# Performance work log

Measured on AMD Instinct MI355X. Metric: run time of the kernel, lower is better.

The kernel has to match this reference:

```python
import jax, jax.numpy as jnp
import numpy as np

N, C, T, H, W = 4, 512, 8, 28, 28
CQ, CV = C // 8, C // 2  # 64, 256


def _maxpool222(a):
    # max_pool3d with kernel=stride=(2,2,2), VALID, over (t,h,w) of [n,c,t,h,w]
    return jax.lax.reduce_window(a, -jnp.inf, jax.lax.max,
                                 (1, 1, 2, 2, 2), (1, 1, 2, 2, 2), 'VALID')


def setup_inputs() -> dict:
    key = jax.random.key(0)
    ks = jax.random.split(key, 6)
    s = lambda fan_in: 1.0 / np.sqrt(fan_in)
    return {
        'x':  jax.random.normal(ks[0], (N, C, T, H, W), dtype=jnp.float32),
        'Wq': jax.random.normal(ks[1], (CQ, C), dtype=jnp.float32) * s(C),
        'Wk': jax.random.normal(ks[2], (CQ, C), dtype=jnp.float32) * s(C),
        'Wv': jax.random.normal(ks[3], (CV, C), dtype=jnp.float32) * s(C),
        'Wz': jax.random.normal(ks[4], (C, CV), dtype=jnp.float32) * s(CV),
        'y':  jax.random.normal(ks[5], (), dtype=jnp.float32) * 0.1,
    }


def reference(x, Wq, Wk, Wv, Wz, y):
    n, c, t, h, w = x.shape
    # 1x1x1 convs (no bias) = per-voxel channel mixing
    q = jnp.einsum('ncthw,oc->nothw', x, Wq)          # [n, CQ, t, h, w]
    k = _maxpool222(jnp.einsum('ncthw,oc->nothw', x, Wk))  # [n, CQ, t/2, h/2, w/2]
    v = _maxpool222(jnp.einsum('ncthw,oc->nothw', x, Wv))  # [n, CV, t/2, h/2, w/2]

    Lq = t * h * w
    Lk = k.shape[2] * k.shape[3] * k.shape[4]
    qf = q.reshape(n, q.shape[1], Lq)                 # [n, CQ, Lq]
    kf = k.reshape(n, k.shape[1], Lk)                 # [n, CQ, Lk]
    vf = v.reshape(n, v.shape[1], Lk)                 # [n, CV, Lk]

    # beta = softmax(q^T k) over kv axis (NOTE: no 1/sqrt(d) scaling, as in source)
    beta = jax.nn.softmax(jnp.einsum('ncq,nck->nqk', qf, kf), axis=-1)  # [n, Lq, Lk]
    att = jnp.einsum('nck,nqk->ncq', vf, beta)        # [n, CV, Lq]
    att = att.reshape(n, vf.shape[1], t, h, w)

    z = jnp.einsum('ncthw,oc->nothw', att, Wz)        # [n, C, t, h, w]
    return y * z + x
```

## Files before the change

### kernel.cpp

```cpp
#include <hip/hip_runtime.h>
#include <hip/hip_bf16.h>

#define LSP  6272
#define LK   784
#define CIN  512
#define CQo  64
#define CVo  256
#define NB   4

typedef __bf16  bf16x8 __attribute__((ext_vector_type(8)));
typedef __bf16  bf16x4 __attribute__((ext_vector_type(4)));
typedef float   f32x4  __attribute__((ext_vector_type(4)));

#define LDT  40

__global__ __launch_bounds__(256) void xt_kernel(const float* __restrict__ x,
                                                 __bf16* __restrict__ xT)
{
    __shared__ __attribute__((aligned(16))) __bf16 tile[64][68];
    int t = threadIdx.x;
    int p0 = blockIdx.x * 64, c0 = blockIdx.y * 64, n = blockIdx.z;
    #pragma unroll
    for (int i = 0; i < 4; i++) {
        int idx = i * 256 + t;
        int c = idx >> 4, p4 = (idx & 15) * 4;
        const float4 v = *reinterpret_cast<const float4*>(
            &x[((size_t)(n * CIN + c0 + c)) * LSP + p0 + p4]);
        tile[p4 + 0][c] = (__bf16)v.x;
        tile[p4 + 1][c] = (__bf16)v.y;
        tile[p4 + 2][c] = (__bf16)v.z;
        tile[p4 + 3][c] = (__bf16)v.w;
    }
    __syncthreads();
    #pragma unroll
    for (int i = 0; i < 4; i++) {
        int idx = i * 256 + t;
        int p = idx >> 4, c4 = (idx & 15) * 4;
        bf16x4 o;
        o[0] = tile[p][c4 + 0]; o[1] = tile[p][c4 + 1];
        o[2] = tile[p][c4 + 2]; o[3] = tile[p][c4 + 3];
        *reinterpret_cast<bf16x4*>(&xT[((size_t)(n * LSP + p0 + p)) * CIN + c0 + c4]) = o;
    }
}

__global__ void wprep_kernel(const float* __restrict__ Wq, const float* __restrict__ Wk,
                             const float* __restrict__ Wv, const float* __restrict__ Wz,
                             __bf16* __restrict__ Wqkv, __bf16* __restrict__ Wzb)
{
    int idx = blockIdx.x * 256 + threadIdx.x;
    if (idx < 384 * 512) {
        int o = idx >> 9;
        float v = (o < 64) ? Wq[idx] : (o < 128) ? Wk[idx - 64 * 512] : Wv[idx - 128 * 512];
        Wqkv[idx] = (__bf16)v;
    }
    if (idx < 512 * 256) Wzb[idx] = (__bf16)Wz[idx];
}

__global__ __launch_bounds__(256) void qkv_gemm(const __bf16* __restrict__ Wqkv,
                                                const __bf16* __restrict__ xT,
                                                __bf16* __restrict__ qT,
                                                __bf16* __restrict__ kT,
                                                __bf16* __restrict__ vconv)
{
    __shared__ __attribute__((aligned(16))) __bf16 As[128 * LDT];
    __shared__ __attribute__((aligned(16))) __bf16 Bs[128 * LDT];
    int t = threadIdx.x;
    int p0 = blockIdx.x * 128;
    int m0 = blockIdx.y * 128;
    int n  = blockIdx.z;
    int lane = t & 63, wid = t >> 6;
    int wm = wid >> 1, wn = wid & 1;
    int lm = lane & 15, lk = lane >> 4;

    f32x4 acc[4][4] = {};

    for (int kb = 0; kb < CIN; kb += 32) {
        #pragma unroll
        for (int i = 0; i < 2; i++) {
            int idx = i * 2048 + t * 8;
            int r = idx >> 5, k8 = idx & 31;
            *reinterpret_cast<uint4*>(&As[r * LDT + k8]) =
                *reinterpret_cast<const uint4*>(&Wqkv[(size_t)(m0 + r) * CIN + kb + k8]);
            *reinterpret_cast<uint4*>(&Bs[r * LDT + k8]) =
                *reinterpret_cast<const uint4*>(&xT[((size_t)(n * LSP + p0 + r)) * CIN + kb + k8]);
        }
        __syncthreads();
        bf16x8 a[4], b[4];
        #pragma unroll
        for (int mi = 0; mi < 4; mi++)
            a[mi] = *reinterpret_cast<const bf16x8*>(&As[(wm * 64 + mi * 16 + lm) * LDT + lk * 8]);
        #pragma unroll
        for (int ni = 0; ni < 4; ni++)
            b[ni] = *reinterpret_cast<const bf16x8*>(&Bs[(wn * 64 + ni * 16 + lm) * LDT + lk * 8]);
        #pragma unroll
        for (int mi = 0; mi < 4; mi++)
            #pragma unroll
            for (int ni = 0; ni < 4; ni++)
                acc[mi][ni] = __builtin_amdgcn_mfma_f32_16x16x32_bf16(a[mi], b[ni], acc[mi][ni], 0, 0, 0);
        __syncthreads();
    }

    #pragma unroll
    for (int mi = 0; mi < 4; mi++) {
        int mloc = wm * 64 + mi * 16 + lk * 4;
        #pragma unroll
        for (int ni = 0; ni < 4; ni++) {
            int p = p0 + wn * 64 + ni * 16 + lm;
            if (m0 == 0) {
                bf16x4 o;
                o[0] = (__bf16)acc[mi][ni][0]; o[1] = (__bf16)acc[mi][ni][1];
                o[2] = (__bf16)acc[mi][ni][2]; o[3] = (__bf16)acc[mi][ni][3];
                if (mloc < 64)
                    *reinterpret_cast<bf16x4*>(&qT[((size_t)(n * LSP + p)) * 64 + mloc]) = o;
                else
                    *reinterpret_cast<bf16x4*>(&kT[((size_t)(n * LSP + p)) * 64 + (mloc - 64)]) = o;
            } else {
                int cv = m0 - 128 + mloc;
                #pragma unroll
                for (int r = 0; r < 4; r++)
                    vconv[((size_t)(n * CVo + cv + r)) * LSP + p] = (__bf16)acc[mi][ni][r];
            }
        }
    }
}

__global__ __launch_bounds__(256) void poolk_kernel(const __bf16* __restrict__ kT,
                                                    __bf16* __restrict__ kpT)
{
    int wid = threadIdx.x >> 6, lane = threadIdx.x & 63;
    int row = blockIdx.x * 4 + wid;
    int n = row / LK, pk = row % LK;
    int tp = pk / 196, rem = pk % 196, hp = rem / 14, wp = rem % 14;
    const __bf16* b = kT + ((size_t)n * LSP + tp * 2 * 784 + hp * 2 * 28 + wp * 2) * 64 + lane;
    float m =        (float)b[0];
    m = fmaxf(m, (float)b[64]);
    m = fmaxf(m, (float)b[28 * 64]);
    m = fmaxf(m, (float)b[29 * 64]);
    m = fmaxf(m, (float)b[784 * 64]);
    m = fmaxf(m, (float)b[785 * 64]);
    m = fmaxf(m, (float)b[812 * 64]);
    m = fmaxf(m, (float)b[813 * 64]);
    kpT[(size_t)row * 64 + lane] = (__bf16)m;
}

__global__ void poolv_kernel(const __bf16* __restrict__ vconv, __bf16* __restrict__ vp)
{
    int id = blockIdx.x * 256 + threadIdx.x;
    if (id >= NB * CVo * LK) return;
    int nc = id / LK, pk = id % LK;
    int tp = pk / 196, rem = pk % 196, hp = rem / 14, wp = rem % 14;
    const __bf16* b = vconv + (size_t)nc * LSP + tp * 2 * 784 + hp * 2 * 28 + wp * 2;
    float m =        (float)b[0];
    m = fmaxf(m, (float)b[1]);   m = fmaxf(m, (float)b[28]);  m = fmaxf(m, (float)b[29]);
    m = fmaxf(m, (float)b[784]); m = fmaxf(m, (float)b[785]); m = fmaxf(m, (float)b[812]); m = fmaxf(m, (float)b[813]);
    vp[id] = (__bf16)m;
}

__global__ __launch_bounds__(256) void flash_kernel(
    const __bf16* __restrict__ qT, const __bf16* __restrict__ kpT,
    const __bf16* __restrict__ vp, __bf16* __restrict__ attT)
{
    __shared__ __attribute__((aligned(16))) __bf16 Ps[64 * 128];
    __shared__ float smem_s[64];
    int t = threadIdx.x;
    int lane = t & 63, w = t >> 6;
    int lm = lane & 15, lk = lane >> 4;
    int q0 = blockIdx.x * 64;
    int n  = blockIdx.y;

    bf16x8 qa[2];
    {
        const __bf16* qrow = &qT[((size_t)(n * LSP + q0 + w * 16 + lm)) * 64 + lk * 8];
        qa[0] = *reinterpret_cast<const bf16x8*>(qrow);
        qa[1] = *reinterpret_cast<const bf16x8*>(qrow + 32);
    }

    f32x4 accO[4][4] = {};
    float m[4], l[4];
    #pragma unroll
    for (int r = 0; r < 4; r++) { m[r] = -1e30f; l[r] = 0.0f; }

    int qrow = w * 16 + lk * 4;

    for (int kt = 0; kt < 7; kt++) {
        int k0 = kt * 128;
        f32x4 accS[8] = {};
        #pragma unroll
        for (int ks = 0; ks < 2; ks++) {
            #pragma unroll
            for (int ni = 0; ni < 8; ni++) {
                int k = k0 + ni * 16 + lm; if (k > 783) k = 783;
                bf16x8 kb = *reinterpret_cast<const bf16x8*>(
                    &kpT[((size_t)(n * LK + k)) * 64 + ks * 32 + lk * 8]);
                accS[ni] = __builtin_amdgcn_mfma_f32_16x16x32_bf16(qa[ks], kb, accS[ni], 0, 0, 0);
            }
        }
        if (kt == 6) {
            #pragma unroll
            for (int ni = 1; ni < 8; ni++)
                #pragma unroll
                for (int r = 0; r < 4; r++) accS[ni][r] = -1e30f;
        }
        float scale[4], lt[4];
        #pragma unroll
        for (int r = 0; r < 4; r++) {
            float v = accS[0][r];
            #pragma unroll
            for (int ni = 1; ni < 8; ni++) v = fmaxf(v, accS[ni][r]);
            #pragma unroll
            for (int d = 1; d < 16; d <<= 1) v = fmaxf(v, __shfl_xor(v, d));
            float mn = fmaxf(m[r], v);
            scale[r] = __expf(m[r] - mn);
            m[r] = mn;
            lt[r] = 0.0f;
        }
        #pragma unroll
        for (int ni = 0; ni < 8; ni++)
            #pragma unroll
            for (int r = 0; r < 4; r++) {
                float p = __expf(accS[ni][r] - m[r]);
                lt[r] += p;
                int q = qrow + r;
                int kl = ni * 16 + lm;
                Ps[q * 128 + (kl ^ ((q & 7) << 3))] = (__bf16)p;
            }
        #pragma unroll
        for (int r = 0; r < 4; r++) {
            #pragma unroll
            for (int d = 1; d < 16; d <<= 1) lt[r] += __shfl_xor(lt[r], d);
            l[r] = l[r] * scale[r] + lt[r];
        }
        if (lm == 0) {
            #pragma unroll
            for (int r = 0; r < 4; r++) smem_s[qrow + r] = scale[r];
        }
        __syncthreads();
        #pragma unroll
        for (int ni = 0; ni < 4; ni++) {
            float s = smem_s[ni * 16 + lm];
            #pragma unroll
            for (int mi = 0; mi < 4; mi++)
                #pragma unroll
                for (int r = 0; r < 4; r++) accO[mi][ni][r] *= s;
        }
        #pragma unroll
        for (int ks = 0; ks < 4; ks++) {
            int kg = k0 + ks * 32 + lk * 8; if (kg > 776) kg = 776;
            bf16x8 pb[4];
            #pragma unroll
            for (int ni = 0; ni < 4; ni++) {
                int q = ni * 16 + lm;
                pb[ni] = *reinterpret_cast<const bf16x8*>(
                    &Ps[q * 128 + ((ks * 32 + lk * 8) ^ ((q & 7) << 3))]);
            }
            #pragma unroll
            for (int mi = 0; mi < 4; mi++) {
                int cv = w * 64 + mi * 16 + lm;
                bf16x8 va = *reinterpret_cast<const bf16x8*>(
                    &vp[((size_t)(n * CVo + cv)) * LK + kg]);
                #pragma unroll
                for (int ni = 0; ni < 4; ni++)
                    accO[mi][ni] = __builtin_amdgcn_mfma_f32_16x16x32_bf16(va, pb[ni], accO[mi][ni], 0, 0, 0);
            }
        }
        __syncthreads();
    }
    if (lm == 0) {
        #pragma unroll
        for (int r = 0; r < 4; r++) smem_s[qrow + r] = 1.0f / l[r];
    }
    __syncthreads();
    #pragma unroll
    for (int ni = 0; ni < 4; ni++) {
        float inv = smem_s[ni * 16 + lm];
        int q = q0 + ni * 16 + lm;
        #pragma unroll
        for (int mi = 0; mi < 4; mi++) {
            bf16x4 o;
            #pragma unroll
            for (int r = 0; r < 4; r++) o[r] = (__bf16)(accO[mi][ni][r] * inv);
            *reinterpret_cast<bf16x4*>(
                &attT[((size_t)(n * LSP + q)) * CVo + w * 64 + mi * 16 + lk * 4]) = o;
        }
    }
}

__global__ __launch_bounds__(256) void z_gemm(const __bf16* __restrict__ Wzb,
                                              const __bf16* __restrict__ attT,
                                              const float* __restrict__ x,
                                              const float* __restrict__ yp,
                                              float* __restrict__ out)
{
    __shared__ __attribute__((aligned(16))) __bf16 As[128 * LDT];
    __shared__ __attribute__((aligned(16))) __bf16 Bs[128 * LDT];
    int t = threadIdx.x;
    int p0 = blockIdx.x * 128;
    int c0 = blockIdx.y * 128;
    int n  = blockIdx.z;
    int lane = t & 63, wid = t >> 6;
    int wm = wid >> 1, wn = wid & 1;
    int lm = lane & 15, lk = lane >> 4;

    f32x4 acc[4][4] = {};

    for (int kb = 0; kb < CVo; kb += 32) {
        #pragma unroll
        for (int i = 0; i < 2; i++) {
            int idx = i * 2048 + t * 8;
            int r = idx >> 5, k8 = idx & 31;
            *reinterpret_cast<uint4*>(&As[r * LDT + k8]) =
                *reinterpret_cast<const uint4*>(&attT[((size_t)(n * LSP + p0 + r)) * CVo + kb + k8]);
            *reinterpret_cast<uint4*>(&Bs[r * LDT + k8]) =
                *reinterpret_cast<const uint4*>(&Wzb[(size_t)(c0 + r) * CVo + kb + k8]);
        }
        __syncthreads();
        bf16x8 a[4], b[4];
        #pragma unroll
        for (int mi = 0; mi < 4; mi++)
            a[mi] = *reinterpret_cast<const bf16x8*>(&As[(wm * 64 + mi * 16 + lm) * LDT + lk * 8]);
        #pragma unroll
        for (int ni = 0; ni < 4; ni++)
            b[ni] = *reinterpret_cast<const bf16x8*>(&Bs[(wn * 64 + ni * 16 + lm) * LDT + lk * 8]);
        #pragma unroll
        for (int mi = 0; mi < 4; mi++)
            #pragma unroll
            for (int ni = 0; ni < 4; ni++)
                acc[mi][ni] = __builtin_amdgcn_mfma_f32_16x16x32_bf16(a[mi], b[ni], acc[mi][ni], 0, 0, 0);
        __syncthreads();
    }

    float yv = yp[0];
    #pragma unroll
    for (int mi = 0; mi < 4; mi++) {
        int p = p0 + wm * 64 + mi * 16 + lk * 4;
        #pragma unroll
        for (int ni = 0; ni < 4; ni++) {
            int c = c0 + wn * 64 + ni * 16 + lm;
            size_t o = ((size_t)(n * CIN + c)) * LSP + p;
            const float4 xv = *reinterpret_cast<const float4*>(&x[o]);
            float4 ov;
            ov.x = yv * acc[mi][ni][0] + xv.x;
            ov.y = yv * acc[mi][ni][1] + xv.y;
            ov.z = yv * acc[mi][ni][2] + xv.z;
            ov.w = yv * acc[mi][ni][3] + xv.w;
            *reinterpret_cast<float4*>(&out[o]) = ov;
        }
    }
}

extern "C" void kernel_launch(void* const* d_in, const int* in_sizes, int n_in,
                              void* d_out, int out_size, void* d_ws, size_t ws_size,
                              hipStream_t stream)
{
    const float* x  = (const float*)d_in[0];
    const float* Wq = (const float*)d_in[1];
    const float* Wk = (const float*)d_in[2];
    const float* Wv = (const float*)d_in[3];
    const float* Wz = (const float*)d_in[4];
    const float* y  = (const float*)d_in[5];
    float* out = (float*)d_out;
    __bf16* ws = (__bf16*)d_ws;

    __bf16* xT    = ws;
    __bf16* kT    = ws + (size_t)12845056;
    __bf16* vconv = ws + (size_t)14450688;
    __bf16* qT    = ws + (size_t)20873216;
    __bf16* kpT   = ws + (size_t)22478848;
    __bf16* vp    = ws + (size_t)22679552;
    __bf16* attT  = ws + (size_t)23482368;
    __bf16* Wqkv  = ws + (size_t)29904896;
    __bf16* Wzb   = ws + (size_t)30101504;

    xt_kernel    <<<dim3(98, 8, 4), 256, 0, stream>>>(x, xT);
    wprep_kernel <<<dim3(768), 256, 0, stream>>>(Wq, Wk, Wv, Wz, Wqkv, Wzb);
    qkv_gemm     <<<dim3(49, 3, 4), 256, 0, stream>>>(Wqkv, xT, qT, kT, vconv);
    poolk_kernel <<<dim3(784), 256, 0, stream>>>(kT, kpT);
    poolv_kernel <<<dim3(3136), 256, 0, stream>>>(vconv, vp);
    flash_kernel <<<dim3(98, 4), 256, 0, stream>>>(qT, kpT, vp, attT);
    z_gemm       <<<dim3(49, 4, 4), 256, 0, stream>>>(Wzb, attT, x, y, out);
}
```

Before: 244.9 us.

## Fuse x transpose into QKV GEMM and rewrite flash attention as single-wave blocks

Drops the separate fp32-to-bf16 transpose kernel: the QKV GEMM now reads x directly, converting and transposing it into swizzled shared memory. For the V output it swaps operand roles so vconv is written with vectorized stores. The flash kernel becomes one wave per block covering 16 queries and 64-key tiles, with a lazy rescale that only fires when the running max grows by more than 8. It also computes S transposed, so the per-row reduction needs only two shuffles, and it removes block-wide syncs. In exchange the V operand is reloaded from global memory by four times as many blocks, and each wave holds 16 accumulator tiles, which raises register pressure.

```diff
diff --git a/kernel.cpp b/kernel.cpp
--- a/kernel.cpp
+++ b/kernel.cpp
@@ -14,35 +14,6 @@
 
 #define LDT  40
 
-__global__ __launch_bounds__(256) void xt_kernel(const float* __restrict__ x,
-                                                 __bf16* __restrict__ xT)
-{
-    __shared__ __attribute__((aligned(16))) __bf16 tile[64][68];
-    int t = threadIdx.x;
-    int p0 = blockIdx.x * 64, c0 = blockIdx.y * 64, n = blockIdx.z;
-    #pragma unroll
-    for (int i = 0; i < 4; i++) {
-        int idx = i * 256 + t;
-        int c = idx >> 4, p4 = (idx & 15) * 4;
-        const float4 v = *reinterpret_cast<const float4*>(
-            &x[((size_t)(n * CIN + c0 + c)) * LSP + p0 + p4]);
-        tile[p4 + 0][c] = (__bf16)v.x;
-        tile[p4 + 1][c] = (__bf16)v.y;
-        tile[p4 + 2][c] = (__bf16)v.z;
-        tile[p4 + 3][c] = (__bf16)v.w;
-    }
-    __syncthreads();
-    #pragma unroll
-    for (int i = 0; i < 4; i++) {
-        int idx = i * 256 + t;
-        int p = idx >> 4, c4 = (idx & 15) * 4;
-        bf16x4 o;
-        o[0] = tile[p][c4 + 0]; o[1] = tile[p][c4 + 1];
-        o[2] = tile[p][c4 + 2]; o[3] = tile[p][c4 + 3];
-        *reinterpret_cast<bf16x4*>(&xT[((size_t)(n * LSP + p0 + p)) * CIN + c0 + c4]) = o;
-    }
-}
-
 __global__ void wprep_kernel(const float* __restrict__ Wq, const float* __restrict__ Wk,
                              const float* __restrict__ Wv, const float* __restrict__ Wz,
                              __bf16* __restrict__ Wqkv, __bf16* __restrict__ Wzb)
@@ -57,7 +28,7 @@
 }
 
 __global__ __launch_bounds__(256) void qkv_gemm(const __bf16* __restrict__ Wqkv,
-                                                const __bf16* __restrict__ xT,
+                                                const float* __restrict__ x,
                                                 __bf16* __restrict__ qT,
                                                 __bf16* __restrict__ kT,
                                                 __bf16* __restrict__ vconv)
@@ -71,6 +42,7 @@
     int lane = t & 63, wid = t >> 6;
     int wm = wid >> 1, wn = wid & 1;
     int lm = lane & 15, lk = lane >> 4;
+    int cS = t >> 3, pqS = t & 7;
 
     f32x4 acc[4][4] = {};
 
@@ -81,32 +53,62 @@
             int r = idx >> 5, k8 = idx & 31;
             *reinterpret_cast<uint4*>(&As[r * LDT + k8]) =
                 *reinterpret_cast<const uint4*>(&Wqkv[(size_t)(m0 + r) * CIN + kb + k8]);
-            *reinterpret_cast<uint4*>(&Bs[r * LDT + k8]) =
-                *reinterpret_cast<const uint4*>(&xT[((size_t)(n * LSP + p0 + r)) * CIN + kb + k8]);
+        }
+        #pragma unroll
+        for (int i = 0; i < 4; i++) {
+            int p = i * 32 + pqS * 4;
+            const float4 v = *reinterpret_cast<const float4*>(
+                &x[((size_t)(n * CIN + kb + cS)) * LSP + p0 + p]);
+            int csw = cS ^ ((pqS & 3) << 3);
+            Bs[(p + 0) * LDT + csw] = (__bf16)v.x;
+            Bs[(p + 1) * LDT + csw] = (__bf16)v.y;
+            Bs[(p + 2) * LDT + csw] = (__bf16)v.z;
+            Bs[(p + 3) * LDT + csw] = (__bf16)v.w;
         }
         __syncthreads();
-        bf16x8 a[4], b[4];
-        #pragma unroll
-        for (int mi = 0; mi < 4; mi++)
-            a[mi] = *reinterpret_cast<const bf16x8*>(&As[(wm * 64 + mi * 16 + lm) * LDT + lk * 8]);
-        #pragma unroll
-        for (int ni = 0; ni < 4; ni++)
-            b[ni] = *reinterpret_cast<const bf16x8*>(&Bs[(wn * 64 + ni * 16 + lm) * LDT + lk * 8]);
-        #pragma unroll
-        for (int mi = 0; mi < 4; mi++)
+        if (m0 == 0) {
+            bf16x8 a[4], b[4];
+            #pragma unroll
+            for (int mi = 0; mi < 4; mi++)
+                a[mi] = *reinterpret_cast<const bf16x8*>(&As[(wm * 64 + mi * 16 + lm) * LDT + lk * 8]);
+            #pragma unroll
+            for (int ni = 0; ni < 4; ni++) {
+                int row = wn * 64 + ni * 16 + lm;
+                b[ni] = *reinterpret_cast<const bf16x8*>(
+                    &Bs[row * LDT + ((lk * 8) ^ (((row >> 2) & 3) << 3))]);
+            }
+            #pragma unroll
+            for (int mi = 0; mi < 4; mi++)
+                #pragma unroll
+                for (int ni = 0; ni < 4; ni++)
+                    acc[mi][ni] = __builtin_amdgcn_mfma_f32_16x16x32_bf16(a[mi], b[ni], acc[mi][ni], 0, 0, 0);
+        } else {
+            bf16x8 a[4], b[4];
+            #pragma unroll
+            for (int mi = 0; mi < 4; mi++) {
+                int row = wn * 64 + mi * 16 + lm;
+                a[mi] = *reinterpret_cast<const bf16x8*>(
+                    &Bs[row * LDT + ((lk * 8) ^ (((row >> 2) & 3) << 3))]);
+            }
             #pragma unroll
             for (int ni = 0; ni < 4; ni++)
-                acc[mi][ni] = __builtin_amdgcn_mfma_f32_16x16x32_bf16(a[mi], b[ni], acc[mi][ni], 0, 0, 0);
+                b[ni] = *reinterpret_cast<const bf16x8*>(&As[(wm * 64 + ni * 16 + lm) * LDT + lk * 8]);
+            #pragma unroll
+            for (int mi = 0; mi < 4; mi++)
+                #pragma unroll
+                for (int ni = 0; ni < 4; ni++)
+                    acc[mi][ni] = __builtin_amdgcn_mfma_f32_16x16x32_bf16(a[mi], b[ni], acc[mi][ni], 0, 0, 0);
+        }
         __syncthreads();
     }
 
-    #pragma unroll
-    for (int mi = 0; mi < 4; mi++) {
-        int mloc = wm * 64 + mi * 16 + lk * 4;
-        #pragma unroll
-        for (int ni = 0; ni < 4; ni++) {
-            int p = p0 + wn * 64 + ni * 16 + lm;
-            if (m0 == 0) {
+    if (m0 == 0) {
+        #pragma unroll
+        for (int mi = 0; mi < 4; mi++) {
+            int mloc = wm * 64 + mi * 16 + lk * 4;
+            #pragma unroll
+            for (int ni = 0; ni < 4; ni++) {
+                int p = p0 + wn * 64 + ni * 16 + lm;
                 bf16x4 o;
                 o[0] = (__bf16)acc[mi][ni][0]; o[1] = (__bf16)acc[mi][ni][1];
                 o[2] = (__bf16)acc[mi][ni][2]; o[3] = (__bf16)acc[mi][ni][3];
@@ -114,11 +116,19 @@
                     *reinterpret_cast<bf16x4*>(&qT[((size_t)(n * LSP + p)) * 64 + mloc]) = o;
                 else
                     *reinterpret_cast<bf16x4*>(&kT[((size_t)(n * LSP + p)) * 64 + (mloc - 64)]) = o;
-            } else {
-                int cv = m0 - 128 + mloc;
-                #pragma unroll
-                for (int r = 0; r < 4; r++)
-                    vconv[((size_t)(n * CVo + cv + r)) * LSP + p] = (__bf16)acc[mi][ni][r];
+            }
+        }
+    } else {
+        #pragma unroll
+        for (int mi = 0; mi < 4; mi++) {
+            int p = p0 + wn * 64 + mi * 16 + lk * 4;
+            #pragma unroll
+            for (int ni = 0; ni < 4; ni++) {
+                int cv = (m0 - 128) + wm * 64 + ni * 16 + lm;
+                bf16x4 o;
+                o[0] = (__bf16)acc[mi][ni][0]; o[1] = (__bf16)acc[mi][ni][1];
+                o[2] = (__bf16)acc[mi][ni][2]; o[3] = (__bf16)acc[mi][ni][3];
+                *reinterpret_cast<bf16x4*>(&vconv[((size_t)(n * CVo + cv)) * LSP + p]) = o;
             }
         }
     }
@@ -156,132 +166,107 @@
     vp[id] = (__bf16)m;
 }
 
-__global__ __launch_bounds__(256) void flash_kernel(
+__global__ __launch_bounds__(64, 2) void flash2_kernel(
     const __bf16* __restrict__ qT, const __bf16* __restrict__ kpT,
     const __bf16* __restrict__ vp, __bf16* __restrict__ attT)
 {
-    __shared__ __attribute__((aligned(16))) __bf16 Ps[64 * 128];
-    __shared__ float smem_s[64];
-    int t = threadIdx.x;
-    int lane = t & 63, w = t >> 6;
+    __shared__ __attribute__((aligned(16))) __bf16 Ps[16 * 64];
+    int lane = threadIdx.x;
     int lm = lane & 15, lk = lane >> 4;
-    int q0 = blockIdx.x * 64;
+    int q0 = blockIdx.x * 16;
     int n  = blockIdx.y;
+    int swz = (lm & 7) << 3;
 
     bf16x8 qa[2];
     {
-        const __bf16* qrow = &qT[((size_t)(n * LSP + q0 + w * 16 + lm)) * 64 + lk * 8];
+        const __bf16* qrow = &qT[((size_t)(n * LSP + q0 + lm)) * 64 + lk * 8];
         qa[0] = *reinterpret_cast<const bf16x8*>(qrow);
         qa[1] = *reinterpret_cast<const bf16x8*>(qrow + 32);
     }
 
-    f32x4 accO[4][4] = {};
-    float m[4], l[4];
+    const __bf16* kbase = kpT + (size_t)n * LK * 64;
+    const __bf16* vbase = vp + (size_t)n * CVo * LK;
+
+    f32x4 accO[16] = {};
+    float m = -1e30f, l = 0.0f;
+
+    for (int kt = 0; kt < 13; kt++) {
+        int kb = kt * 64;
+        bool last = (kb == 768);
+        int nkg = last ? 1 : 4;
+        f32x4 accS[4] = {};
+        #pragma unroll
+        for (int kg = 0; kg < 4; kg++) {
+            if (kg < nkg) {
+                #pragma unroll
+                for (int ks = 0; ks < 2; ks++) {
+                    bf16x8 kf = *reinterpret_cast<const bf16x8*>(
+                        &kbase[((size_t)(kb + kg * 16 + lm)) * 64 + ks * 32 + lk * 8]);
+                    accS[kg] = __builtin_amdgcn_mfma_f32_16x16x32_bf16(kf, qa[ks], accS[kg], 0, 0, 0);
+                }
+            }
+        }
+        float v = -1e30f;
+        #pragma unroll
+        for (int kg = 0; kg < 4; kg++)
+            if (kg < nkg)
+                #pragma unroll
+                for (int r = 0; r < 4; r++) v = fmaxf(v, accS[kg][r]);
+        v = fmaxf(v, __shfl_xor(v, 16));
+        v = fmaxf(v, __shfl_xor(v, 32));
+        float mn = fmaxf(m, v);
+        if (__any(mn - m > 8.0f)) {
+            float scale = __expf(m - mn);
+            m = mn;
+            l *= scale;
+            #pragma unroll
+            for (int mi = 0; mi < 16; mi++)
+                #pragma unroll
+                for (int r = 0; r < 4; r++) accO[mi][r] *= scale;
+        }
+        float lt = 0.0f;
+        #pragma unroll
+        for (int kg = 0; kg < 4; kg++) {
+            bf16x4 pw;
+            if (kg < nkg) {
+                #pragma unroll
+                for (int r = 0; r < 4; r++) {
+                    float p = __expf(accS[kg][r] - m);
+                    lt += p;
+                    pw[r] = (__bf16)p;
+                }
+            } else {
+                pw[0] = (__bf16)0.f; pw[1] = (__bf16)0.f; pw[2] = (__bf16)0.f; pw[3] = (__bf16)0.f;
+            }
+            if (kg < 2 || !last)
+                *reinterpret_cast<bf16x4*>(&Ps[lm * 64 + ((kg * 16 + lk * 4) ^ swz)]) = pw;
+        }
+        lt += __shfl_xor(lt, 16);
+        lt += __shfl_xor(lt, 32);
+        l += lt;
+        int nks = last ? 1 : 2;
+        #pragma unroll
+        for (int ks = 0; ks < 2; ks++) {
+            if (ks < nks) {
+                bf16x8 pf = *reinterpret_cast<const bf16x8*>(
+                    &Ps[lm * 64 + ((ks * 32 + lk * 8) ^ swz)]);
+                const __bf16* vk = &vbase[(size_t)lm * LK + kb + ks * 32 + lk * 8];
+                #pragma unroll
+                for (int mi = 0; mi < 16; mi++) {
+                    bf16x8 vf = *reinterpret_cast<const bf16x8*>(&vk[(size_t)(mi * 16) * LK]);
+                    accO[mi] = __builtin_amdgcn_mfma_f32_16x16x32_bf16(vf, pf, accO[mi], 0, 0, 0);
+                }
+            }
+        }
+    }
+    float inv = 1.0f / l;
+    __bf16* orow = &attT[((size_t)(n * LSP + q0 + lm)) * CVo + lk * 4];
     #pragma unroll
-    for (int r = 0; r < 4; r++) { m[r] = -1e30f; l[r] = 0.0f; }
-
-    int qrow = w * 16 + lk * 4;
-
-    for (int kt = 0; kt < 7; kt++) {
-        int k0 = kt * 128;
-        f32x4 accS[8] = {};
-        #pragma unroll
-        for (int ks = 0; ks < 2; ks++) {
-            #pragma unroll
-            for (int ni = 0; ni < 8; ni++) {
-                int k = k0 + ni * 16 + lm; if (k > 783) k = 783;
-                bf16x8 kb = *reinterpret_cast<const bf16x8*>(
-                    &kpT[((size_t)(n * LK + k)) * 64 + ks * 32 + lk * 8]);
-                accS[ni] = __builtin_amdgcn_mfma_f32_16x16x32_bf16(qa[ks], kb, accS[ni], 0, 0, 0);
-            }
-        }
-        if (kt == 6) {
-            #pragma unroll
-            for (int ni = 1; ni < 8; ni++)
-                #pragma unroll
-                for (int r = 0; r < 4; r++) accS[ni][r] = -1e30f;
-        }
-        float scale[4], lt[4];
-        #pragma unroll
-        for (int r = 0; r < 4; r++) {
-            float v = accS[0][r];
-            #pragma unroll
-            for (int ni = 1; ni < 8; ni++) v = fmaxf(v, accS[ni][r]);
-            #pragma unroll
-            for (int d = 1; d < 16; d <<= 1) v = fmaxf(v, __shfl_xor(v, d));
-            float mn = fmaxf(m[r], v);
-            scale[r] = __expf(m[r] - mn);
-            m[r] = mn;
-            lt[r] = 0.0f;
-        }
-        #pragma unroll
-        for (int ni = 0; ni < 8; ni++)
-            #pragma unroll
-            for (int r = 0; r < 4; r++) {
-                float p = __expf(accS[ni][r] - m[r]);
-                lt[r] += p;
-                int q = qrow + r;
-                int kl = ni * 16 + lm;
-                Ps[q * 128 + (kl ^ ((q & 7) << 3))] = (__bf16)p;
-            }
-        #pragma unroll
-        for (int r = 0; r < 4; r++) {
-            #pragma unroll
-            for (int d = 1; d < 16; d <<= 1) lt[r] += __shfl_xor(lt[r], d);
-            l[r] = l[r] * scale[r] + lt[r];
-        }
-        if (lm == 0) {
-            #pragma unroll
-            for (int r = 0; r < 4; r++) smem_s[qrow + r] = scale[r];
-        }
-        __syncthreads();
-        #pragma unroll
-        for (int ni = 0; ni < 4; ni++) {
-            float s = smem_s[ni * 16 + lm];
-            #pragma unroll
-            for (int mi = 0; mi < 4; mi++)
-                #pragma unroll
-                for (int r = 0; r < 4; r++) accO[mi][ni][r] *= s;
-        }
-        #pragma unroll
-        for (int ks = 0; ks < 4; ks++) {
-            int kg = k0 + ks * 32 + lk * 8; if (kg > 776) kg = 776;
-            bf16x8 pb[4];
-            #pragma unroll
-            for (int ni = 0; ni < 4; ni++) {
-                int q = ni * 16 + lm;
-                pb[ni] = *reinterpret_cast<const bf16x8*>(
-                    &Ps[q * 128 + ((ks * 32 + lk * 8) ^ ((q & 7) << 3))]);
-            }
-            #pragma unroll
-            for (int mi = 0; mi < 4; mi++) {
-                int cv = w * 64 + mi * 16 + lm;
-                bf16x8 va = *reinterpret_cast<const bf16x8*>(
-                    &vp[((size_t)(n * CVo + cv)) * LK + kg]);
-                #pragma unroll
-                for (int ni = 0; ni < 4; ni++)
-                    accO[mi][ni] = __builtin_amdgcn_mfma_f32_16x16x32_bf16(va, pb[ni], accO[mi][ni], 0, 0, 0);
-            }
-        }
-        __syncthreads();
-    }
-    if (lm == 0) {
-        #pragma unroll
-        for (int r = 0; r < 4; r++) smem_s[qrow + r] = 1.0f / l[r];
-    }
-    __syncthreads();
-    #pragma unroll
-    for (int ni = 0; ni < 4; ni++) {
-        float inv = smem_s[ni * 16 + lm];
-        int q = q0 + ni * 16 + lm;
-        #pragma unroll
-        for (int mi = 0; mi < 4; mi++) {
-            bf16x4 o;
-            #pragma unroll
-            for (int r = 0; r < 4; r++) o[r] = (__bf16)(accO[mi][ni][r] * inv);
-            *reinterpret_cast<bf16x4*>(
-                &attT[((size_t)(n * LSP + q)) * CVo + w * 64 + mi * 16 + lk * 4]) = o;
-        }
+    for (int mi = 0; mi < 16; mi++) {
+        bf16x4 o;
+        o[0] = (__bf16)(accO[mi][0] * inv); o[1] = (__bf16)(accO[mi][1] * inv);
+        o[2] = (__bf16)(accO[mi][2] * inv); o[3] = (__bf16)(accO[mi][3] * inv);
+        *reinterpret_cast<bf16x4*>(&orow[mi * 16]) = o;
     }
 }
 
@@ -361,21 +346,19 @@
     float* out = (float*)d_out;
     __bf16* ws = (__bf16*)d_ws;
 
-    __bf16* xT    = ws;
-    __bf16* kT    = ws + (size_t)12845056;
-    __bf16* vconv = ws + (size_t)14450688;
-    __bf16* qT    = ws + (size_t)20873216;
-    __bf16* kpT   = ws + (size_t)22478848;
-    __bf16* vp    = ws + (size_t)22679552;
-    __bf16* attT  = ws + (size_t)23482368;
-    __bf16* Wqkv  = ws + (size_t)29904896;
-    __bf16* Wzb   = ws + (size_t)30101504;
-
-    xt_kernel    <<<dim3(98, 8, 4), 256, 0, stream>>>(x, xT);
-    wprep_kernel <<<dim3(768), 256, 0, stream>>>(Wq, Wk, Wv, Wz, Wqkv, Wzb);
-    qkv_gemm     <<<dim3(49, 3, 4), 256, 0, stream>>>(Wqkv, xT, qT, kT, vconv);
-    poolk_kernel <<<dim3(784), 256, 0, stream>>>(kT, kpT);
-    poolv_kernel <<<dim3(3136), 256, 0, stream>>>(vconv, vp);
-    flash_kernel <<<dim3(98, 4), 256, 0, stream>>>(qT, kpT, vp, attT);
-    z_gemm       <<<dim3(49, 4, 4), 256, 0, stream>>>(Wzb, attT, x, y, out);
-}
+    __bf16* kT    = ws;
+    __bf16* vconv = ws + (size_t)1605632;
+    __bf16* qT    = ws + (size_t)8028160;
+    __bf16* kpT   = ws + (size_t)9633792;
+    __bf16* vp    = ws + (size_t)9834496;
+    __bf16* attT  = ws + (size_t)10637312;
+    __bf16* Wqkv  = ws + (size_t)17059840;
+    __bf16* Wzb   = ws + (size_t)17256448;
+
+    wprep_kernel  <<<dim3(768), 256, 0, stream>>>(Wq, Wk, Wv, Wz, Wqkv, Wzb);
+    qkv_gemm      <<<dim3(49, 3, 4), 256, 0, stream>>>(Wqkv, x, qT, kT, vconv);
+    poolk_kernel  <<<dim3(784), 256, 0, stream>>>(kT, kpT);
+    poolv_kernel  <<<dim3(3136), 256, 0, stream>>>(vconv, vp);
+    flash2_kernel <<<dim3(392, 4), 64, 0, stream>>>(qT, kpT, vp, attT);
+    z_gemm        <<<dim3(49, 4, 4), 256, 0, stream>>>(Wzb, attT, x, y, out);
+}
```

Result: slower. 299.1 us (+22.1%).
